# Kernel tuning notes

Hardware: AMD Instinct MI355X
Metric: run time of the kernel (lower is better)

The kernel has to match this reference:

```python
import jax, jax.numpy as jnp
import numpy as np

D_MODEL = 1024
H = 16
D_FF = 2048
EPS = 1e-5


def _ln(x, g, b):
    m = jnp.mean(x, axis=-1, keepdims=True)
    v = jnp.mean((x - m) ** 2, axis=-1, keepdims=True)
    return (x - m) * jax.lax.rsqrt(v + EPS) * g + b


def setup_inputs() -> dict:
    key = jax.random.key(0)
    ks = jax.random.split(key, 16)
    d, dff = D_MODEL, D_FF
    s = 1.0 / np.sqrt(d)
    inp = {
        "x": jax.random.normal(ks[0], (2, 2048, d), jnp.float32),
        "Wq": jax.random.normal(ks[1], (d, d), jnp.float32) * s,
        "bq": jax.random.normal(ks[2], (d,), jnp.float32) * 0.01,
        "Wk": jax.random.normal(ks[3], (d, d), jnp.float32) * s,
        "bk": jax.random.normal(ks[4], (d,), jnp.float32) * 0.01,
        "Wv": jax.random.normal(ks[5], (d, d), jnp.float32) * s,
        "bv": jax.random.normal(ks[6], (d,), jnp.float32) * 0.01,
        "Wo": jax.random.normal(ks[7], (d, d), jnp.float32) * s,
        "bo": jax.random.normal(ks[8], (d,), jnp.float32) * 0.01,
        "ln1_g": 1.0 + 0.1 * jax.random.normal(ks[9], (d,), jnp.float32),
        "ln1_b": 0.01 * jax.random.normal(ks[10], (d,), jnp.float32),
        "ln2_g": 1.0 + 0.1 * jax.random.normal(ks[11], (d,), jnp.float32),
        "ln2_b": 0.01 * jax.random.normal(ks[12], (d,), jnp.float32),
        "W1": jax.random.normal(ks[13], (d, dff), jnp.float32) * s,
        "b1": 0.01 * jax.random.normal(ks[14], (dff,), jnp.float32),
        "W2": jax.random.normal(ks[15], (dff, d), jnp.float32) * (1.0 / np.sqrt(dff)),
        "b2": jnp.zeros((d,), jnp.float32),
    }
    return inp


def reference(x, Wq, bq, Wk, bk, Wv, bv, Wo, bo, ln1_g, ln1_b, ln2_g, ln2_b, W1, b1, W2, b2):
    b, s, d = x.shape
    dk = d // H

    # --- sublayer 1: pre-LN self-attention with residual (dropout = eval/identity) ---
    y = _ln(x, ln1_g, ln1_b)
    q = (y @ Wq + bq).reshape(b, s, H, dk).transpose(0, 2, 1, 3)  # (b,h,s,dk)
    k = (y @ Wk + bk).reshape(b, s, H, dk).transpose(0, 2, 1, 3)
    v = (y @ Wv + bv).reshape(b, s, H, dk).transpose(0, 2, 1, 3)
    scores = jnp.einsum("bhqd,bhkd->bhqk", q, k) / jnp.sqrt(jnp.float32(dk))
    attn = jax.nn.softmax(scores, axis=-1)
    o = jnp.einsum("bhqk,bhkd->bhqd", attn, v)  # (b,h,s,dk)
    # faithful to original bug: transpose last two dims then flat reshape
    o = jnp.swapaxes(o, -1, -2).reshape(b, s, d)  # (b,h,dk,s) -> (b,s,d)
    x = x + (o @ Wo + bo)

    # --- sublayer 2: pre-LN FFN with residual ---
    y2 = _ln(x, ln2_g, ln2_b)
    f = jax.nn.relu(y2 @ W1 + b1) @ W2 + b2
    return x + f
```

## Files before the change

### kernel.cpp

```cpp
#include <hip/hip_runtime.h>
#include <hip/hip_bf16.h>

#define D_MODEL 1024
#define NHEAD 16
#define DK 64
#define DFF 2048
#define SEQ 2048
#define NBATCH 2
#define NTOK (NBATCH*SEQ)

typedef __attribute__((ext_vector_type(8))) short bf16x8;
typedef __attribute__((ext_vector_type(4))) float f32x4;
typedef __attribute__((ext_vector_type(16))) float f32x16;
typedef __attribute__((ext_vector_type(4))) short s16x4;

#if __has_builtin(__builtin_amdgcn_exp2f)
#define EXP2(x) __builtin_amdgcn_exp2f(x)
#else
#define EXP2(x) exp2f(x)
#endif

__device__ __forceinline__ short f2bf(float f) {
    union { float f; unsigned u; } v; v.f = f;
    unsigned r = v.u + 0x7FFFu + ((v.u >> 16) & 1u);
    return (short)(r >> 16);
}

__device__ __forceinline__ void gld16(void* lds, const void* g) {
    __builtin_amdgcn_global_load_lds(
        (const __attribute__((address_space(1))) void*)g,
        (__attribute__((address_space(3))) void*)lds, 16, 0, 0);
}

__global__ __launch_bounds__(256) void k_transpose(const float* __restrict__ W,
                                                   short* __restrict__ WT, int K, int N)
{
    __shared__ float t[32][33];
    int tid = threadIdx.x;
    int n0 = blockIdx.x * 32, k0 = blockIdx.y * 32;
#pragma unroll
    for (int p = 0; p < 4; ++p) {
        int idx = p * 256 + tid, r = idx >> 5, c = idx & 31;
        t[r][c] = W[(size_t)(k0 + r) * N + (n0 + c)];
    }
    __syncthreads();
#pragma unroll
    for (int p = 0; p < 4; ++p) {
        int idx = p * 256 + tid, r = idx >> 5, c = idx & 31;
        WT[(size_t)(n0 + r) * K + (k0 + c)] = f2bf(t[c][r]);
    }
}

struct TP4 { const float* src[4]; short* dst[4]; };
__global__ __launch_bounds__(256) void k_transpose4(TP4 tp)
{
    __shared__ float t[32][33];
    const float* W = tp.src[blockIdx.z];
    short* WT = tp.dst[blockIdx.z];
    const int K = 1024, N = 1024;
    int tid = threadIdx.x;
    int n0 = blockIdx.x * 32, k0 = blockIdx.y * 32;
#pragma unroll
    for (int p = 0; p < 4; ++p) {
        int idx = p * 256 + tid, r = idx >> 5, c = idx & 31;
        t[r][c] = W[(size_t)(k0 + r) * N + (n0 + c)];
    }
    __syncthreads();
#pragma unroll
    for (int p = 0; p < 4; ++p) {
        int idx = p * 256 + tid, r = idx >> 5, c = idx & 31;
        WT[(size_t)(n0 + r) * K + (k0 + c)] = f2bf(t[c][r]);
    }
}

__global__ __launch_bounds__(256) void k_layernorm(const float* __restrict__ x,
                                                   const float* __restrict__ g,
                                                   const float* __restrict__ bta,
                                                   short* __restrict__ y)
{
    int row = blockIdx.x * 4 + (threadIdx.x >> 6);
    int lane = threadIdx.x & 63;
    const float* xr = x + (size_t)row * D_MODEL;
    float4 v[4];
    float s = 0.f, s2 = 0.f;
#pragma unroll
    for (int c = 0; c < 4; ++c) {
        v[c] = *(const float4*)(xr + c * 256 + lane * 4);
        s  += v[c].x + v[c].y + v[c].z + v[c].w;
        s2 += v[c].x * v[c].x + v[c].y * v[c].y + v[c].z * v[c].z + v[c].w * v[c].w;
    }
#pragma unroll
    for (int off = 1; off < 64; off <<= 1) {
        s  += __shfl_xor(s, off, 64);
        s2 += __shfl_xor(s2, off, 64);
    }
    float mean = s * (1.f / 1024.f);
    float var  = s2 * (1.f / 1024.f) - mean * mean;
    float rs = rsqrtf(var + 1e-5f);
    short* yr = y + (size_t)row * D_MODEL;
#pragma unroll
    for (int c = 0; c < 4; ++c) {
        int idx = c * 256 + lane * 4;
        float4 gg = *(const float4*)(g + idx);
        float4 bb = *(const float4*)(bta + idx);
        s16x4 o;
        o.x = f2bf((v[c].x - mean) * rs * gg.x + bb.x);
        o.y = f2bf((v[c].y - mean) * rs * gg.y + bb.y);
        o.z = f2bf((v[c].z - mean) * rs * gg.z + bb.z);
        o.w = f2bf((v[c].w - mean) * rs * gg.w + bb.w);
        *(s16x4*)(yr + idx) = o;
    }
}

template<int EPI, int BN, int THREADS>
__global__ __launch_bounds__(THREADS) void k_gemm(
    const short* __restrict__ A, const short* __restrict__ BT, int N, int K,
    const float* __restrict__ bias, const float* __restrict__ bias2, const float* __restrict__ bias3,
    const float* __restrict__ resid, float* __restrict__ outF,
    short* __restrict__ outB, short* __restrict__ outQ, short* __restrict__ outK, short* __restrict__ outV)
{
    constexpr int CW = THREADS / 128;
    __shared__ __align__(16) short sA[3][128 * 32];
    __shared__ __align__(16) short sB[3][BN * 32];
    int tid = threadIdx.x;
    int lane = tid & 63, wid = tid >> 6;
    int wr = wid / CW, wc = wid % CW;
    int lrow = lane & 15;
    int lk16 = (lane >> 4) << 4;

    int gx = gridDim.x;
    int nwg = gx * gridDim.y;
    int orig = blockIdx.x + blockIdx.y * gx;
    int wg = (orig & 7) * (nwg >> 3) + (orig >> 3);
    int bx = wg % gx, by = wg / gx;

    const short* Ab = A + (size_t)by * 128 * K;
    const short* Bb = BT + (size_t)bx * BN * K;

    auto src = [&](const short* base, int cc) {
        int r = cc >> 2, s = cc & 3;
        return (const char*)(base + (size_t)r * K) + (((s ^ ((r >> 1) & 3)) << 4));
    };
    const char *pA0, *pA1 = nullptr, *pB0;
    pA0 = src(Ab, tid);
    pB0 = src(Bb, tid & (BN * 4 - 1));
    if constexpr (THREADS == 256) pA1 = src(Ab, 256 + tid);

    auto stage = [&](int buf) {
        if constexpr (THREADS == 512) {
            gld16(&sA[buf][tid * 8], pA0);  pA0 += 64;
            gld16(&sB[buf][tid * 8], pB0);  pB0 += 64;
        } else {
            gld16(&sA[buf][tid * 8], pA0);          pA0 += 64;
            gld16(&sA[buf][(256 + tid) * 8], pA1);  pA1 += 64;
            gld16(&sB[buf][(tid & (BN * 4 - 1)) * 8], pB0);  pB0 += 64;
        }
    };
    constexpr int LPS = (THREADS == 512) ? 2 : 3;

    const f32x4 fz = {0.f, 0.f, 0.f, 0.f};
    f32x4 acc[4][2];
#pragma unroll
    for (int i = 0; i < 4; i++)
#pragma unroll
        for (int j = 0; j < 2; j++) acc[i][j] = fz;

    const int NT = K / 32;
    stage(0);
    stage(1);
    int cur = 0;
    for (int t = 0; t < NT; ++t) {
        if (t + 2 < NT) {
            int nb3 = cur + 2; if (nb3 >= 3) nb3 -= 3;
            stage(nb3);
            if constexpr (LPS == 2) asm volatile("s_waitcnt vmcnt(4)" ::: "memory");
            else                    asm volatile("s_waitcnt vmcnt(6)" ::: "memory");
        } else if (t + 1 < NT) {
            if constexpr (LPS == 2) asm volatile("s_waitcnt vmcnt(2)" ::: "memory");
            else                    asm volatile("s_waitcnt vmcnt(3)" ::: "memory");
        } else {
            asm volatile("s_waitcnt vmcnt(0)" ::: "memory");
        }
        __builtin_amdgcn_s_barrier();
        bf16x8 af[4], bfr[2];
#pragma unroll
        for (int i = 0; i < 4; i++) {
            int row = wr * 64 + i * 16 + lrow;
            af[i] = *(const bf16x8*)((const char*)sA[cur] + row * 64 + (lk16 ^ (((row >> 1) & 3) << 4)));
        }
#pragma unroll
        for (int j = 0; j < 2; j++) {
            int row = wc * 32 + j * 16 + lrow;
            bfr[j] = *(const bf16x8*)((const char*)sB[cur] + row * 64 + (lk16 ^ (((row >> 1) & 3) << 4)));
        }
#pragma unroll
        for (int i = 0; i < 4; i++)
#pragma unroll
            for (int j = 0; j < 2; j++)
                acc[i][j] = __builtin_amdgcn_mfma_f32_16x16x32_bf16(af[i], bfr[j], acc[i][j], 0, 0, 0);
        __builtin_amdgcn_s_barrier();
        ++cur; if (cur >= 3) cur = 0;
    }

    int m_base = by * 128 + wr * 64 + (lane >> 4) * 4;
    int n_base = bx * BN + wc * 32 + lrow;
#pragma unroll
    for (int i = 0; i < 4; i++) {
#pragma unroll
        for (int j = 0; j < 2; j++) {
            int n = n_base + j * 16;
#pragma unroll
            for (int jj = 0; jj < 4; jj++) {
                int m = m_base + i * 16 + jj;
                float v = acc[i][j][jj];
                if constexpr (EPI == 0) {
                    int seg = n >> 10, nn = n & 1023;
                    int b = m >> 11, ss = m & 2047;
                    int h = nn >> 6, dd = nn & 63;
                    if (seg == 0) {
                        outQ[(((size_t)(b * NHEAD + h)) * SEQ + ss) * DK + dd] =
                            f2bf((v + bias[nn]) * 0.18033688011112042f);
                    } else if (seg == 1) {
                        outK[(((size_t)(b * NHEAD + h)) * SEQ + ss) * DK + dd] = f2bf(v + bias2[nn]);
                    } else {
                        outV[(((size_t)(b * NHEAD + h)) * DK + dd) * SEQ + ss] = f2bf(v + bias3[nn]);
                    }
                } else if constexpr (EPI == 1) {
                    size_t idx = (size_t)m * N + n;
                    outF[idx] = v + bias[n] + resid[idx];
                } else if constexpr (EPI == 2) {
                    float r2 = v + bias[n];
                    outB[(size_t)m * N + n] = f2bf(r2 > 0.f ? r2 : 0.f);
                } else {
                    size_t idx = (size_t)m * N + n;
                    outF[idx] = v + bias[n] + resid[idx];
                }
            }
        }
    }
}

__global__ __launch_bounds__(256) void k_attn(const short* __restrict__ Q, const short* __restrict__ Kk,
                                              const short* __restrict__ Vt, short* __restrict__ Operm)
{
    __shared__ __align__(16) short sMem[2][2][64 * 64];
    int tid = threadIdx.x, lane = tid & 63;
    int wid = tid >> 6;
    int qg = wid >> 1, ks = wid & 1;
    int l31 = lane & 31, hi = lane >> 5;

    int orig = blockIdx.x + blockIdx.y * 32;
    int lg = (orig & 7) * 128 + (orig >> 3);
    int bh = lg >> 5, qt = lg & 31;
    int b = bh >> 4, h = bh & 15;
    int q0 = qt * 64 + qg * 32;
    const short* Qp = Q + (size_t)bh * SEQ * DK;
    const short* Kp = Kk + (size_t)bh * SEQ * DK;
    const short* Vp = Vt + (size_t)bh * DK * SEQ;

    bf16x8 qf[4];
#pragma unroll
    for (int kb = 0; kb < 4; ++kb)
        qf[kb] = *(const bf16x8*)(Qp + (size_t)(q0 + l31) * DK + kb * 16 + hi * 8);

    int c0 = tid, c1 = 256 + tid;
    int r0 = c0 >> 3, r1 = c1 >> 3;
    const char* pK0 = (const char*)(Kp + (size_t)r0 * DK) + (((c0 & 7) ^ (r0 & 7)) << 4);
    const char* pK1 = (const char*)(Kp + (size_t)r1 * DK) + (((c1 & 7) ^ (r1 & 7)) << 4);
    const char* pV0 = (const char*)(Vp + (size_t)r0 * SEQ) + (((c0 & 7) ^ (r0 & 7)) << 4);
    const char* pV1 = (const char*)(Vp + (size_t)r1 * SEQ) + (((c1 & 7) ^ (r1 & 7)) << 4);

    auto stage = [&](int buf) {
        gld16(&sMem[buf][0][c0 * 8], pK0);  pK0 += 8192;
        gld16(&sMem[buf][0][c1 * 8], pK1);  pK1 += 8192;
        gld16(&sMem[buf][1][c0 * 8], pV0);  pV0 += 128;
        gld16(&sMem[buf][1][c1 * 8], pV1);  pV1 += 128;
    };

    f32x16 Oa0 = {0,0,0,0,0,0,0,0,0,0,0,0,0,0,0,0};
    f32x16 Oa1 = {0,0,0,0,0,0,0,0,0,0,0,0,0,0,0,0};
    float lsum = 0.f;

    stage(0);
    const int NT = SEQ / 64;
    int krow = ks * 32 + l31;
    int sw = (l31 & 7) << 4;
    for (int t = 0; t < NT; ++t) {
        int cur = t & 1;
        if (t + 1 < NT) {
            stage(cur ^ 1);
            asm volatile("s_waitcnt vmcnt(4)" ::: "memory");
        } else {
            asm volatile("s_waitcnt vmcnt(0)" ::: "memory");
        }
        __builtin_amdgcn_s_barrier();
        const char* sKc = (const char*)sMem[cur][0];
        const char* sVc = (const char*)sMem[cur][1];

        f32x16 sc = {0,0,0,0,0,0,0,0,0,0,0,0,0,0,0,0};
#pragma unroll
        for (int kb = 0; kb < 4; ++kb) {
            int cb = (kb * 32 + hi * 16) ^ sw;
            bf16x8 kf = *(const bf16x8*)(sKc + krow * 128 + cb);
            sc = __builtin_amdgcn_mfma_f32_32x32x16_bf16(kf, qf[kb], sc, 0, 0, 0);
        }

        unsigned W[4][2];
#pragma unroll
        for (int tt = 0; tt < 4; ++tt) {
            float pa_ = EXP2(sc[4*tt+0]), pb_ = EXP2(sc[4*tt+1]);
            float pc_ = EXP2(sc[4*tt+2]), pd_ = EXP2(sc[4*tt+3]);
            lsum += (pa_ + pb_) + (pc_ + pd_);
            asm("v_cvt_pk_bf16_f32 %0, %1, %2" : "=v"(W[tt][0]) : "v"(pa_), "v"(pb_));
            asm("v_cvt_pk_bf16_f32 %0, %1, %2" : "=v"(W[tt][1]) : "v"(pc_), "v"(pd_));
        }

        auto pv_step = [&](unsigned a0, unsigned a1, unsigned b0v, unsigned b1v, int kslice) {
            asm("v_permlane32_swap_b32 %0, %1" : "+v"(a0), "+v"(b0v));
            asm("v_permlane32_swap_b32 %0, %1" : "+v"(a1), "+v"(b1v));
            union { unsigned u[4]; bf16x8 v; } pa;
            pa.u[0] = a0; pa.u[1] = a1; pa.u[2] = b0v; pa.u[3] = b1v;
            int cb = (kslice * 32 + hi * 16) ^ sw;
            bf16x8 vf0 = *(const bf16x8*)(sVc + l31 * 128 + cb);
            bf16x8 vf1 = *(const bf16x8*)(sVc + (32 + l31) * 128 + cb);
            Oa0 = __builtin_amdgcn_mfma_f32_32x32x16_bf16(pa.v, vf0, Oa0, 0, 0, 0);
            Oa1 = __builtin_amdgcn_mfma_f32_32x32x16_bf16(pa.v, vf1, Oa1, 0, 0, 0);
        };
        pv_step(W[0][0], W[0][1], W[1][0], W[1][1], ks * 2 + 0);
        pv_step(W[2][0], W[2][1], W[3][0], W[3][1], ks * 2 + 1);
        __builtin_amdgcn_s_barrier();
    }

    lsum += __shfl_xor(lsum, 32, 64);

    float* mrg = (float*)sMem;
    if (ks == 1) {
        float* m0 = mrg + (qg * 64 + lane) * 33;
#pragma unroll
        for (int i = 0; i < 16; ++i) m0[i] = Oa0[i];
#pragma unroll
        for (int i = 0; i < 16; ++i) m0[16 + i] = Oa1[i];
        m0[32] = lsum;
    }
    __syncthreads();
    if (ks == 0) {
        const float* m0 = mrg + (qg * 64 + lane) * 33;
#pragma unroll
        for (int i = 0; i < 16; ++i) Oa0[i] += m0[i];
#pragma unroll
        for (int i = 0; i < 16; ++i) Oa1[i] += m0[16 + i];
        lsum += m0[32];

        float rlv[16];
#pragma unroll
        for (int tt = 0; tt < 4; ++tt)
#pragma unroll
            for (int rr = 0; rr < 4; ++rr) {
                float ts = __shfl(lsum, 4 * hi + 8 * tt + rr, 64);
                rlv[4 * tt + rr] = 1.f / ts;
            }

        int qcol = (q0 & 1023) + 4 * hi;
        int qhi = q0 >> 10;
#pragma unroll
        for (int db = 0; db < 2; ++db) {
            const f32x16& O = db ? Oa1 : Oa0;
            int dd = db * 32 + l31;
            size_t rowoff = ((size_t)b * SEQ + h * 128 + 2 * dd + qhi) * D_MODEL + qcol;
#pragma unroll
            for (int tt = 0; tt < 4; ++tt) {
                s16x4 o;
                o.x = f2bf(O[4*tt+0] * rlv[4*tt+0]);
                o.y = f2bf(O[4*tt+1] * rlv[4*tt+1]);
                o.z = f2bf(O[4*tt+2] * rlv[4*tt+2]);
                o.w = f2bf(O[4*tt+3] * rlv[4*tt+3]);
                *(s16x4*)(Operm + rowoff + 8 * tt) = o;
            }
        }
    }
}

extern "C" void kernel_launch(void* const* d_in, const int* in_sizes, int n_in,
                              void* d_out, int out_size, void* d_ws, size_t ws_size,
                              hipStream_t stream)
{
    const float* x   = (const float*)d_in[0];
    const float* Wq  = (const float*)d_in[1];
    const float* bq  = (const float*)d_in[2];
    const float* Wk  = (const float*)d_in[3];
    const float* bk  = (const float*)d_in[4];
    const float* Wv  = (const float*)d_in[5];
    const float* bv  = (const float*)d_in[6];
    const float* Wo  = (const float*)d_in[7];
    const float* bo  = (const float*)d_in[8];
    const float* g1  = (const float*)d_in[9];
    const float* b1l = (const float*)d_in[10];
    const float* g2  = (const float*)d_in[11];
    const float* b2l = (const float*)d_in[12];
    const float* W1  = (const float*)d_in[13];
    const float* b1  = (const float*)d_in[14];
    const float* W2  = (const float*)d_in[15];
    const float* b2  = (const float*)d_in[16];
    float* out = (float*)d_out;

    char* ws = (char*)d_ws;
    size_t off = 0;
    auto alloc = [&](size_t bytes) {
        char* p = ws + off;
        off += (bytes + 255) & ~(size_t)255;
        return p;
    };
    short* WqkvT = (short*)alloc((size_t)3072 * 1024 * 2);
    short* WoT   = (short*)alloc((size_t)1024 * 1024 * 2);
    short* W1T   = (short*)alloc((size_t)2048 * 1024 * 2);
    short* W2T   = (short*)alloc((size_t)1024 * 2048 * 2);
    short* Y     = (short*)alloc((size_t)NTOK * 1024 * 2);
    short* Qb    = (short*)alloc((size_t)NTOK * 1024 * 2);
    short* Kb    = (short*)alloc((size_t)NTOK * 1024 * 2);
    short* Vtb   = (short*)alloc((size_t)NTOK * 1024 * 2);
    short* Operm = (short*)alloc((size_t)NTOK * 1024 * 2);
    float* X1    = (float*)alloc((size_t)NTOK * 1024 * 4);
    short* F1    = (short*)alloc((size_t)NTOK * 2048 * 2);

    TP4 tp;
    tp.src[0] = Wq; tp.dst[0] = WqkvT;
    tp.src[1] = Wk; tp.dst[1] = WqkvT + 1024 * 1024;
    tp.src[2] = Wv; tp.dst[2] = WqkvT + 2048 * 1024;
    tp.src[3] = Wo; tp.dst[3] = WoT;
    k_transpose4<<<dim3(32, 32, 4), 256, 0, stream>>>(tp);
    k_transpose<<<dim3(64, 32), 256, 0, stream>>>(W1, W1T, 1024, 2048);
    k_transpose<<<dim3(32, 64), 256, 0, stream>>>(W2, W2T, 2048, 1024);

    k_layernorm<<<NTOK / 4, 256, 0, stream>>>(x, g1, b1l, Y);

    k_gemm<0,128,512><<<dim3(24, 32), 512, 0, stream>>>(Y, WqkvT, 3072, 1024,
        bq, bk, bv, nullptr, nullptr, nullptr, Qb, Kb, Vtb);

    k_attn<<<dim3(32, 32), 256, 0, stream>>>(Qb, Kb, Vtb, Operm);

    k_gemm<1,64,256><<<dim3(16, 32), 256, 0, stream>>>(Operm, WoT, 1024, 1024,
        bo, nullptr, nullptr, x, X1, nullptr, nullptr, nullptr, nullptr);

    k_layernorm<<<NTOK / 4, 256, 0, stream>>>(X1, g2, b2l, Y);

    k_gemm<2,128,512><<<dim3(16, 32), 512, 0, stream>>>(Y, W1T, 2048, 1024,
        b1, nullptr, nullptr, nullptr, nullptr, F1, nullptr, nullptr, nullptr);

    k_gemm<3,64,256><<<dim3(16, 32), 256, 0, stream>>>(F1, W2T, 1024, 2048,
        b2, nullptr, nullptr, X1, out, nullptr, nullptr, nullptr, nullptr);
}
```

Baseline: 199.1 us.

## Compute softmax row sums via MFMA with ones, add setprio and unroll attention loop

The attention kernel now accumulates the softmax denominator by multiplying the bf16 probabilities with a vector of ones on the matrix unit, so the per-lane scalar sums and the cross-lane shuffles at the end go away. The merge buffer grows to hold these sums. MFMA blocks are wrapped in s_setprio and the tile loop is unrolled by two so buffer indices are constant. The GEMM gets a min-waves launch bound and interleaves the A-fragment loads with the MFMAs. Trade-offs are an extra MFMA per PV step, sums taken from bf16-rounded probabilities, and the register limit the launch bound imposes on the GEMM.

```diff
diff --git a/kernel.cpp b/kernel.cpp
--- a/kernel.cpp
+++ b/kernel.cpp
@@ -113,13 +113,13 @@
 }
 
 template<int EPI, int BN, int THREADS>
-__global__ __launch_bounds__(THREADS) void k_gemm(
+__global__ __launch_bounds__(THREADS, (THREADS == 512) ? 8 : 4) void k_gemm(
     const short* __restrict__ A, const short* __restrict__ BT, int N, int K,
     const float* __restrict__ bias, const float* __restrict__ bias2, const float* __restrict__ bias3,
     const float* __restrict__ resid, float* __restrict__ outF,
     short* __restrict__ outB, short* __restrict__ outQ, short* __restrict__ outK, short* __restrict__ outV)
 {
-    constexpr int CW = THREADS / 128;
+    constexpr int CW = (THREADS == 512) ? 4 : 2;
     __shared__ __align__(16) short sA[3][128 * 32];
     __shared__ __align__(16) short sB[3][BN * 32];
     int tid = threadIdx.x;
@@ -139,12 +139,15 @@
 
     auto src = [&](const short* base, int cc) {
         int r = cc >> 2, s = cc & 3;
-        return (const char*)(base + (size_t)r * K) + (((s ^ ((r >> 1) & 3)) << 4));
-    };
-    const char *pA0, *pA1 = nullptr, *pB0;
-    pA0 = src(Ab, tid);
-    pB0 = src(Bb, tid & (BN * 4 - 1));
-    if constexpr (THREADS == 256) pA1 = src(Ab, 256 + tid);
+        return (const char*)(base + (size_t)r * K) + ((s ^ ((r >> 1) & 3)) << 4);
+    };
+    const char *pA0 = src(Ab, tid), *pA1 = nullptr, *pB0;
+    if constexpr (THREADS == 512) {
+        pB0 = src(Bb, tid);
+    } else {
+        pA1 = src(Ab, 256 + tid);
+        pB0 = src(Bb, tid & (BN * 4 - 1));
+    }
 
     auto stage = [&](int buf) {
         if constexpr (THREADS == 512) {
@@ -156,7 +159,6 @@
             gld16(&sB[buf][(tid & (BN * 4 - 1)) * 8], pB0);  pB0 += 64;
         }
     };
-    constexpr int LPS = (THREADS == 512) ? 2 : 3;
 
     const f32x4 fz = {0.f, 0.f, 0.f, 0.f};
     f32x4 acc[4][2];
@@ -173,31 +175,28 @@
         if (t + 2 < NT) {
             int nb3 = cur + 2; if (nb3 >= 3) nb3 -= 3;
             stage(nb3);
-            if constexpr (LPS == 2) asm volatile("s_waitcnt vmcnt(4)" ::: "memory");
-            else                    asm volatile("s_waitcnt vmcnt(6)" ::: "memory");
+            if constexpr (THREADS == 512) asm volatile("s_waitcnt vmcnt(4)" ::: "memory");
+            else                          asm volatile("s_waitcnt vmcnt(6)" ::: "memory");
         } else if (t + 1 < NT) {
-            if constexpr (LPS == 2) asm volatile("s_waitcnt vmcnt(2)" ::: "memory");
-            else                    asm volatile("s_waitcnt vmcnt(3)" ::: "memory");
+            if constexpr (THREADS == 512) asm volatile("s_waitcnt vmcnt(2)" ::: "memory");
+            else                          asm volatile("s_waitcnt vmcnt(3)" ::: "memory");
         } else {
             asm volatile("s_waitcnt vmcnt(0)" ::: "memory");
         }
         __builtin_amdgcn_s_barrier();
-        bf16x8 af[4], bfr[2];
-#pragma unroll
-        for (int i = 0; i < 4; i++) {
-            int row = wr * 64 + i * 16 + lrow;
-            af[i] = *(const bf16x8*)((const char*)sA[cur] + row * 64 + (lk16 ^ (((row >> 1) & 3) << 4)));
-        }
+        bf16x8 bfr[2];
 #pragma unroll
         for (int j = 0; j < 2; j++) {
             int row = wc * 32 + j * 16 + lrow;
             bfr[j] = *(const bf16x8*)((const char*)sB[cur] + row * 64 + (lk16 ^ (((row >> 1) & 3) << 4)));
         }
 #pragma unroll
-        for (int i = 0; i < 4; i++)
-#pragma unroll
-            for (int j = 0; j < 2; j++)
-                acc[i][j] = __builtin_amdgcn_mfma_f32_16x16x32_bf16(af[i], bfr[j], acc[i][j], 0, 0, 0);
+        for (int i = 0; i < 4; i++) {
+            int row = wr * 64 + i * 16 + lrow;
+            bf16x8 af = *(const bf16x8*)((const char*)sA[cur] + row * 64 + (lk16 ^ (((row >> 1) & 3) << 4)));
+            acc[i][0] = __builtin_amdgcn_mfma_f32_16x16x32_bf16(af, bfr[0], acc[i][0], 0, 0, 0);
+            acc[i][1] = __builtin_amdgcn_mfma_f32_16x16x32_bf16(af, bfr[1], acc[i][1], 0, 0, 0);
+        }
         __builtin_amdgcn_s_barrier();
         ++cur; if (cur >= 3) cur = 0;
     }
@@ -263,6 +262,9 @@
     for (int kb = 0; kb < 4; ++kb)
         qf[kb] = *(const bf16x8*)(Qp + (size_t)(q0 + l31) * DK + kb * 16 + hi * 8);
 
+    const short one_bf = (short)0x3F80;
+    const bf16x8 onesf = {one_bf, one_bf, one_bf, one_bf, one_bf, one_bf, one_bf, one_bf};
+
     int c0 = tid, c1 = 256 + tid;
     int r0 = c0 >> 3, r1 = c1 >> 3;
     const char* pK0 = (const char*)(Kp + (size_t)r0 * DK) + (((c0 & 7) ^ (r0 & 7)) << 4);
@@ -279,14 +281,27 @@
 
     f32x16 Oa0 = {0,0,0,0,0,0,0,0,0,0,0,0,0,0,0,0};
     f32x16 Oa1 = {0,0,0,0,0,0,0,0,0,0,0,0,0,0,0,0};
-    float lsum = 0.f;
-
-    stage(0);
+    f32x16 Ls  = {0,0,0,0,0,0,0,0,0,0,0,0,0,0,0,0};
+
     const int NT = SEQ / 64;
     int krow = ks * 32 + l31;
     int sw = (l31 & 7) << 4;
-    for (int t = 0; t < NT; ++t) {
-        int cur = t & 1;
+
+    auto pv_step = [&](unsigned a0, unsigned a1, unsigned b0v, unsigned b1v, int kslice,
+                       const char* sVc) {
+        asm("v_permlane32_swap_b32 %0, %1" : "+v"(a0), "+v"(b0v));
+        asm("v_permlane32_swap_b32 %0, %1" : "+v"(a1), "+v"(b1v));
+        union { unsigned u[4]; bf16x8 v; } pa;
+        pa.u[0] = a0; pa.u[1] = a1; pa.u[2] = b0v; pa.u[3] = b1v;
+        int cb = (kslice * 32 + hi * 16) ^ sw;
+        bf16x8 vf0 = *(const bf16x8*)(sVc + l31 * 128 + cb);
+        bf16x8 vf1 = *(const bf16x8*)(sVc + (32 + l31) * 128 + cb);
+        Oa0 = __builtin_amdgcn_mfma_f32_32x32x16_bf16(pa.v, vf0, Oa0, 0, 0, 0);
+        Oa1 = __builtin_amdgcn_mfma_f32_32x32x16_bf16(pa.v, vf1, Oa1, 0, 0, 0);
+        Ls  = __builtin_amdgcn_mfma_f32_32x32x16_bf16(pa.v, onesf, Ls, 0, 0, 0);
+    };
+
+    auto tile = [&](int t, int cur) {
         if (t + 1 < NT) {
             stage(cur ^ 1);
             asm volatile("s_waitcnt vmcnt(4)" ::: "memory");
@@ -298,67 +313,57 @@
         const char* sVc = (const char*)sMem[cur][1];
 
         f32x16 sc = {0,0,0,0,0,0,0,0,0,0,0,0,0,0,0,0};
+        __builtin_amdgcn_s_setprio(1);
 #pragma unroll
         for (int kb = 0; kb < 4; ++kb) {
             int cb = (kb * 32 + hi * 16) ^ sw;
             bf16x8 kf = *(const bf16x8*)(sKc + krow * 128 + cb);
             sc = __builtin_amdgcn_mfma_f32_32x32x16_bf16(kf, qf[kb], sc, 0, 0, 0);
         }
+        __builtin_amdgcn_s_setprio(0);
 
         unsigned W[4][2];
 #pragma unroll
         for (int tt = 0; tt < 4; ++tt) {
             float pa_ = EXP2(sc[4*tt+0]), pb_ = EXP2(sc[4*tt+1]);
             float pc_ = EXP2(sc[4*tt+2]), pd_ = EXP2(sc[4*tt+3]);
-            lsum += (pa_ + pb_) + (pc_ + pd_);
             asm("v_cvt_pk_bf16_f32 %0, %1, %2" : "=v"(W[tt][0]) : "v"(pa_), "v"(pb_));
             asm("v_cvt_pk_bf16_f32 %0, %1, %2" : "=v"(W[tt][1]) : "v"(pc_), "v"(pd_));
         }
 
-        auto pv_step = [&](unsigned a0, unsigned a1, unsigned b0v, unsigned b1v, int kslice) {
-            asm("v_permlane32_swap_b32 %0, %1" : "+v"(a0), "+v"(b0v));
-            asm("v_permlane32_swap_b32 %0, %1" : "+v"(a1), "+v"(b1v));
-            union { unsigned u[4]; bf16x8 v; } pa;
-            pa.u[0] = a0; pa.u[1] = a1; pa.u[2] = b0v; pa.u[3] = b1v;
-            int cb = (kslice * 32 + hi * 16) ^ sw;
-            bf16x8 vf0 = *(const bf16x8*)(sVc + l31 * 128 + cb);
-            bf16x8 vf1 = *(const bf16x8*)(sVc + (32 + l31) * 128 + cb);
-            Oa0 = __builtin_amdgcn_mfma_f32_32x32x16_bf16(pa.v, vf0, Oa0, 0, 0, 0);
-            Oa1 = __builtin_amdgcn_mfma_f32_32x32x16_bf16(pa.v, vf1, Oa1, 0, 0, 0);
-        };
-        pv_step(W[0][0], W[0][1], W[1][0], W[1][1], ks * 2 + 0);
-        pv_step(W[2][0], W[2][1], W[3][0], W[3][1], ks * 2 + 1);
+        __builtin_amdgcn_s_setprio(1);
+        pv_step(W[0][0], W[0][1], W[1][0], W[1][1], ks * 2 + 0, sVc);
+        pv_step(W[2][0], W[2][1], W[3][0], W[3][1], ks * 2 + 1, sVc);
+        __builtin_amdgcn_s_setprio(0);
         __builtin_amdgcn_s_barrier();
-    }
-
-    lsum += __shfl_xor(lsum, 32, 64);
+    };
+
+    stage(0);
+    for (int t = 0; t < NT; t += 2) {
+        tile(t, 0);
+        tile(t + 1, 1);
+    }
 
     float* mrg = (float*)sMem;
     if (ks == 1) {
-        float* m0 = mrg + (qg * 64 + lane) * 33;
+        float* m0 = mrg + (qg * 64 + lane) * 49;
 #pragma unroll
         for (int i = 0; i < 16; ++i) m0[i] = Oa0[i];
 #pragma unroll
         for (int i = 0; i < 16; ++i) m0[16 + i] = Oa1[i];
-        m0[32] = lsum;
+#pragma unroll
+        for (int i = 0; i < 16; ++i) m0[32 + i] = Ls[i];
     }
     __syncthreads();
     if (ks == 0) {
-        const float* m0 = mrg + (qg * 64 + lane) * 33;
+        const float* m0 = mrg + (qg * 64 + lane) * 49;
+        float rlv[16];
 #pragma unroll
         for (int i = 0; i < 16; ++i) Oa0[i] += m0[i];
 #pragma unroll
         for (int i = 0; i < 16; ++i) Oa1[i] += m0[16 + i];
-        lsum += m0[32];
-
-        float rlv[16];
-#pragma unroll
-        for (int tt = 0; tt < 4; ++tt)
-#pragma unroll
-            for (int rr = 0; rr < 4; ++rr) {
-                float ts = __shfl(lsum, 4 * hi + 8 * tt + rr, 64);
-                rlv[4 * tt + rr] = 1.f / ts;
-            }
+#pragma unroll
+        for (int i = 0; i < 16; ++i) rlv[i] = 1.f / (Ls[i] + m0[32 + i]);
 
         int qcol = (q0 & 1023) + 4 * hi;
         int qhi = q0 >> 10;
```

Measured after the change: 199.6 us. No clear change (+0.3%).
